# Performance work log

Hardware: AMD Instinct MI355X
Metric: run time of the kernel (lower is better)

The kernel has to match this reference:

```python
import jax, jax.numpy as jnp
import numpy as np

N, E = 50000, 800000
HID, HEADS, EDIM = 64, 4, 32
HC = HID * HEADS
NEG_SLOPE = 0.2
LN_EPS = 1e-5


def setup_inputs() -> dict:
    key = jax.random.key(0)
    ks = jax.random.split(key, 16)
    s = lambda d: 1.0 / np.sqrt(d)
    return {
        "x": jax.random.normal(ks[0], (N, HID), jnp.float32),
        "edge_index": jax.random.randint(ks[1], (2, E), 0, N, jnp.int64),
        "edge_attr": jax.random.normal(ks[2], (E, EDIM), jnp.float32),
        # GATv2Conv params
        "W_l": jax.random.normal(ks[3], (HID, HC), jnp.float32) * s(HID),
        "b_l": jnp.zeros((HC,), jnp.float32),
        "W_r": jax.random.normal(ks[4], (HID, HC), jnp.float32) * s(HID),
        "b_r": jnp.zeros((HC,), jnp.float32),
        "W_e": jax.random.normal(ks[5], (EDIM, HC), jnp.float32) * s(EDIM),
        "att": jax.random.normal(ks[6], (HEADS, HID), jnp.float32) * s(HID),
        "bias_gat": jnp.zeros((HC,), jnp.float32),
        # block params
        "W1": jax.random.normal(ks[7], (HID, HC), jnp.float32) * s(HID),
        "b1": jnp.zeros((HC,), jnp.float32),
        "gamma": jnp.ones((HC,), jnp.float32),
        "beta": jnp.zeros((HC,), jnp.float32),
        "W2": jax.random.normal(ks[8], (HC, HID), jnp.float32) * s(HC),
        "b2": jnp.zeros((HID,), jnp.float32),
    }


def _gatv2(x, edge_index, edge_attr, W_l, b_l, W_r, b_r, W_e, att, bias_gat):
    src, dst = edge_index[0], edge_index[1]
    x_l = (x @ W_l + b_l).reshape(N, HEADS, HID)  # source transform
    x_r = (x @ W_r + b_r).reshape(N, HEADS, HID)  # target transform
    e = (edge_attr @ W_e).reshape(E, HEADS, HID)
    m = x_l[src] + x_r[dst] + e                    # [E, H, C]
    m = jax.nn.leaky_relu(m, NEG_SLOPE)
    alpha = jnp.einsum('ehc,hc->eh', m, att)       # [E, H]
    # segment softmax over incoming edges of each target node
    amax = jax.ops.segment_max(alpha, dst, num_segments=N)
    alpha = jnp.exp(alpha - amax[dst])
    denom = jax.ops.segment_sum(alpha, dst, num_segments=N)
    alpha = alpha / (denom[dst] + 1e-16)
    out = jax.ops.segment_sum(x_l[src] * alpha[..., None], dst, num_segments=N)
    return out.reshape(N, HC) + bias_gat


def reference(x, edge_index, edge_attr, W_l, b_l, W_r, b_r, W_e, att, bias_gat,
              W1, b1, gamma, beta, W2, b2):
    h = _gatv2(x, edge_index, edge_attr, W_l, b_l, W_r, b_r, W_e, att, bias_gat)
    xl = jnp.tanh(x @ W1 + b1)
    z = xl + h
    mu = jnp.mean(z, axis=-1, keepdims=True)
    var = jnp.var(z, axis=-1, keepdims=True)
    z = (z - mu) * jax.lax.rsqrt(var + LN_EPS) * gamma + beta
    return jnp.tanh(z @ W2 + b2)
```

## Files before the change

kernel.cpp:

```cpp
#include <hip/hip_runtime.h>
#include <math.h>

#define N_NODES 50000
#define N_EDGES 800000
#define HID 64
#define HEADS 4
#define HC 256
#define NEG_SLOPE 0.2f
#define LN_EPS 1e-5f
#define EDGE_BLOCKS 2048

typedef __attribute__((ext_vector_type(8))) short bf16x8;
typedef __attribute__((ext_vector_type(8))) unsigned short u16x8;
typedef __attribute__((ext_vector_type(4))) float f32x4;

__device__ __forceinline__ float bf2f(unsigned short u) {
    return __uint_as_float(((unsigned int)u) << 16);
}
__device__ __forceinline__ unsigned short f2bf(float f) {
    unsigned int u = __float_as_uint(f);
    u = (u + 0x7fffu + ((u >> 16) & 1u)) >> 16;
    return (unsigned short)u;
}
__device__ __forceinline__ float fast_tanh(float v) {
    const float c = fminf(fmaxf(v, -15.f), 15.f);
    const float e = __expf(2.f * c);
    return 1.f - 2.f / (e + 1.f);
}

__global__ __launch_bounds__(256) void k_node_transform(
    const float* __restrict__ x,
    const float* __restrict__ W_l, const float* __restrict__ b_l,
    const float* __restrict__ W_r, const float* __restrict__ b_r,
    unsigned short* __restrict__ xl_t, unsigned short* __restrict__ xr_t)
{
    __shared__ float xs[8][64];
    __shared__ unsigned short tl[8][256], tr[8][256];
    const int n0 = blockIdx.x * 8;
    const int t = threadIdx.x;
    for (int i = t; i < 8 * 64; i += 256) xs[i >> 6][i & 63] = x[n0 * 64 + i];
    __syncthreads();

    float accl[8], accr[8];
    const float bl = b_l[t], br = b_r[t];
#pragma unroll
    for (int n = 0; n < 8; n++) { accl[n] = bl; accr[n] = br; }
    for (int k = 0; k < 64; k++) {
        const float wl = W_l[k * 256 + t];
        const float wr = W_r[k * 256 + t];
#pragma unroll
        for (int n = 0; n < 8; n++) {
            accl[n] = fmaf(xs[n][k], wl, accl[n]);
            accr[n] = fmaf(xs[n][k], wr, accr[n]);
        }
    }
    const int pos = (t & 15) * 16 + (t >> 4);
#pragma unroll
    for (int n = 0; n < 8; n++) {
        tl[n][pos] = f2bf(accl[n]);
        tr[n][pos] = f2bf(accr[n]);
    }
    __syncthreads();
    const int n = t >> 5, q = t & 31;
    ushort4 v0 = *(const ushort4*)&tl[n][q * 8];
    ushort4 v1 = *(const ushort4*)&tl[n][q * 8 + 4];
    ushort4 w0 = *(const ushort4*)&tr[n][q * 8];
    ushort4 w1 = *(const ushort4*)&tr[n][q * 8 + 4];
    *(ushort4*)(xl_t + (size_t)(n0 + n) * 256 + q * 8)     = v0;
    *(ushort4*)(xl_t + (size_t)(n0 + n) * 256 + q * 8 + 4) = v1;
    *(ushort4*)(xr_t + (size_t)(n0 + n) * 256 + q * 8)     = w0;
    *(ushort4*)(xr_t + (size_t)(n0 + n) * 256 + q * 8 + 4) = w1;
}

__global__ __launch_bounds__(256) void k_prep(
    const float* __restrict__ W_e, const float* __restrict__ att,
    unsigned short* __restrict__ wfrag, unsigned short* __restrict__ att_t)
{
    const int t = threadIdx.x;
#pragma unroll
    for (int s = 0; s < 4; s++) {
        const int slot = t * 4 + s;
        const int nt = slot >> 6, ls = slot & 63;
        const int col = nt * 16 + (ls & 15);
        const int kb = (ls >> 4) * 8;
#pragma unroll
        for (int j = 0; j < 8; j++)
            wfrag[slot * 8 + j] = f2bf(W_e[(kb + j) * 256 + col]);
    }
    att_t[t] = f2bf(att[(t & 15) * 16 + (t >> 4)]);
}

__global__ __launch_bounds__(256) void k_hist(const int* __restrict__ ei, int* __restrict__ count)
{
    const int e = blockIdx.x * 256 + threadIdx.x;
    if (e < N_EDGES) atomicAdd(&count[ei[N_EDGES + e]], 1);
}

__global__ __launch_bounds__(1024) void k_scan(const int* __restrict__ count, int* __restrict__ off)
{
    __shared__ int wsum[16];
    __shared__ int s_carry;
    const int t = threadIdx.x, lane = t & 63, wv = t >> 6;
    if (t == 0) s_carry = 0;
    __syncthreads();
    for (int base = 0; base < N_NODES; base += 8192) {
        const int idx0 = base + t * 8;
        int v[8];
#pragma unroll
        for (int j = 0; j < 8; j++) { int i = idx0 + j; v[j] = (i < N_NODES) ? count[i] : 0; }
#pragma unroll
        for (int j = 1; j < 8; j++) v[j] += v[j - 1];
        const int tot = v[7];
        int sc = tot;
#pragma unroll
        for (int s = 1; s < 64; s <<= 1) { int o = __shfl_up(sc, s, 64); if (lane >= s) sc += o; }
        if (lane == 63) wsum[wv] = sc;
        __syncthreads();
        const int carry = s_carry;
        int woff = 0;
        for (int u = 0; u < wv; u++) woff += wsum[u];
        const int ebase = carry + woff + (sc - tot);
#pragma unroll
        for (int j = 0; j < 8; j++) {
            int i = idx0 + j;
            if (i < N_NODES) off[i] = ebase + (j ? v[j - 1] : 0);
        }
        __syncthreads();
        if (t == 0) { int tt = 0; for (int u = 0; u < 16; u++) tt += wsum[u]; s_carry = carry + tt; }
        __syncthreads();
    }
    if (threadIdx.x == 0) off[N_NODES] = s_carry;
}

__global__ __launch_bounds__(256) void k_scatter(
    const int* __restrict__ ei, const int* __restrict__ off, int* __restrict__ cursor,
    const float* __restrict__ edge_attr,
    int* __restrict__ csr_src, unsigned short* __restrict__ ea_csr)
{
    const int e = blockIdx.x * 256 + threadIdx.x;
    if (e < N_EDGES) {
        const int s = ei[e];
        const int d = ei[N_EDGES + e];
        const int pos = off[d] + atomicAdd(&cursor[d], 1);
        csr_src[pos] = s;
        const float4* src4 = (const float4*)(edge_attr + (size_t)e * 32);
        ushort4* dst4 = (ushort4*)(ea_csr + (size_t)pos * 32);
#pragma unroll
        for (int i = 0; i < 8; i++) {
            const float4 v = src4[i];
            ushort4 u;
            u.x = f2bf(v.x); u.y = f2bf(v.y); u.z = f2bf(v.z); u.w = f2bf(v.w);
            dst4[i] = u;
        }
    }
}

template<bool F32>
__global__ __launch_bounds__(256) void k_edgeagg(
    const int* __restrict__ off, const int* __restrict__ csr_src,
    const unsigned short* __restrict__ ea_csr,
    const unsigned short* __restrict__ wfrag, const unsigned short* __restrict__ att_t,
    const unsigned short* __restrict__ xl_t, const unsigned short* __restrict__ xr_t,
    void* __restrict__ zs_g)
{
    __shared__ unsigned short bfrag_s[16][64][8];

    const int t = threadIdx.x;
    const int lane = t & 63, wv = t >> 6;
    const int arow = lane & 15, koct = lane >> 4;

    for (int i = t; i < 1024; i += 256)
        *(u16x8*)&bfrag_s[i >> 6][i & 63][0] = *(const u16x8*)(wfrag + i * 8);
    __syncthreads();

    const u16x8 attL = *(const u16x8*)(att_t + arow * 16);
    const u16x8 attH = *(const u16x8*)(att_t + arow * 16 + 8);

    const int STRIDE = EDGE_BLOCKS * 4;
    int node = blockIdx.x * 4 + wv;
    if (node >= N_NODES) return;

    int lo = off[node], hi = off[node + 1];
    u16x8 xrl = *(const u16x8*)(xr_t + (size_t)node * 256 + arow * 16);
    u16x8 xrh = *(const u16x8*)(xr_t + (size_t)node * 256 + arow * 16 + 8);
    while (hi <= lo) {
#pragma unroll
        for (int q = 0; q < 4; q++) {
            const int nt = koct * 4 + q;
            if (F32) ((float*)zs_g)[(size_t)node * 256 + nt * 16 + arow] = 0.f;
            else ((unsigned short*)zs_g)[(size_t)node * 256 + nt * 16 + arow] = 0;
        }
        node += STRIDE;
        if (node >= N_NODES) return;
        lo = off[node]; hi = off[node + 1];
        xrl = *(const u16x8*)(xr_t + (size_t)node * 256 + arow * 16);
        xrh = *(const u16x8*)(xr_t + (size_t)node * 256 + arow * 16 + 8);
    }
    int nnode = node + STRIDE;
    bool nvalid = nnode < N_NODES;
    int nlo = 0, nhi = 0;
    u16x8 nxrl = xrl, nxrh = xrh;
    if (nvalid) {
        nlo = off[nnode]; nhi = off[nnode + 1];
        nxrl = *(const u16x8*)(xr_t + (size_t)nnode * 256 + arow * 16);
        nxrh = *(const u16x8*)(xr_t + (size_t)nnode * 256 + arow * 16 + 8);
    }
    int p0 = lo;
    bf16x8 af;
    u16x8 xlo[4], xhi[4];
    {
        const int pa = min(p0 + arow, hi - 1);
        const int sv0 = csr_src[pa];
        af = *(const bf16x8*)(ea_csr + (size_t)pa * 32 + koct * 8);
#pragma unroll
        for (int r = 0; r < 4; r++) {
            const int sr = __shfl(sv0, koct * 4 + r, 64);
            const unsigned short* bp = xl_t + (size_t)sr * 256 + arow * 16;
            xlo[r] = *(const u16x8*)bp;
            xhi[r] = *(const u16x8*)(bp + 8);
        }
    }

    float g[16];
#pragma unroll
    for (int i = 0; i < 16; i++) g[i] = 0.f;
    float dsum[4] = {0.f, 0.f, 0.f, 0.f};

    for (;;) {
        const bool last = (p0 + 16 >= hi);
        bool uvalid;
        int up0, uhic;
        if (!last) { uvalid = true; up0 = p0 + 16; uhic = hi; }
        else {
            while (nvalid && nlo >= nhi) {
#pragma unroll
                for (int q = 0; q < 4; q++) {
                    const int nt = koct * 4 + q;
                    if (F32) ((float*)zs_g)[(size_t)nnode * 256 + nt * 16 + arow] = 0.f;
                    else ((unsigned short*)zs_g)[(size_t)nnode * 256 + nt * 16 + arow] = 0;
                }
                nnode += STRIDE;
                nvalid = nnode < N_NODES;
                if (nvalid) {
                    nlo = off[nnode]; nhi = off[nnode + 1];
                    nxrl = *(const u16x8*)(xr_t + (size_t)nnode * 256 + arow * 16);
                    nxrh = *(const u16x8*)(xr_t + (size_t)nnode * 256 + arow * 16 + 8);
                }
            }
            uvalid = nvalid; up0 = nlo; uhic = nhi;
        }
        int usv = 0;
        bf16x8 uaf = af;
        if (uvalid) {
            const int upa = min(up0 + arow, uhic - 1);
            usv = csr_src[upa];
            uaf = *(const bf16x8*)(ea_csr + (size_t)upa * 32 + koct * 8);
        }

        float s_[4][4];
#pragma unroll
        for (int r = 0; r < 4; r++)
#pragma unroll
            for (int h = 0; h < 4; h++) s_[r][h] = 0.f;

#pragma unroll
        for (int nt = 0; nt < 8; nt++) {
            const bf16x8 bfr = *(const bf16x8*)&bfrag_s[nt][lane][0];
            f32x4 dacc = {0.f, 0.f, 0.f, 0.f};
            dacc = __builtin_amdgcn_mfma_f32_16x16x32_bf16(af, bfr, dacc, 0, 0, 0);
            const float xrv = bf2f((unsigned short)xrl[nt]);
            const float atv = bf2f((unsigned short)attL[nt]);
            const int h = nt >> 2;
#pragma unroll
            for (int r = 0; r < 4; r++) {
                const float xv = bf2f((unsigned short)xlo[r][nt]);
                float mm = dacc[r] + xv + xrv;
                mm = (mm > 0.f) ? mm : NEG_SLOPE * mm;
                s_[r][h] = fmaf(atv, mm, s_[r][h]);
            }
        }
        u16x8 uxlo[4], uxhi[4];
        if (uvalid) {
#pragma unroll
            for (int r = 0; r < 4; r++) {
                const int sr = __shfl(usv, koct * 4 + r, 64);
                const unsigned short* bp = xl_t + (size_t)sr * 256 + arow * 16;
                uxlo[r] = *(const u16x8*)bp;
                uxhi[r] = *(const u16x8*)(bp + 8);
            }
        } else {
#pragma unroll
            for (int r = 0; r < 4; r++) { uxlo[r] = xlo[r]; uxhi[r] = xhi[r]; }
        }
#pragma unroll
        for (int n2 = 0; n2 < 8; n2++) {
            const int nt = n2 + 8;
            const bf16x8 bfr = *(const bf16x8*)&bfrag_s[nt][lane][0];
            f32x4 dacc = {0.f, 0.f, 0.f, 0.f};
            dacc = __builtin_amdgcn_mfma_f32_16x16x32_bf16(af, bfr, dacc, 0, 0, 0);
            const float xrv = bf2f((unsigned short)xrh[n2]);
            const float atv = bf2f((unsigned short)attH[n2]);
            const int h = nt >> 2;
#pragma unroll
            for (int r = 0; r < 4; r++) {
                const float xv = bf2f((unsigned short)xhi[r][n2]);
                float mm = dacc[r] + xv + xrv;
                mm = (mm > 0.f) ? mm : NEG_SLOPE * mm;
                s_[r][h] = fmaf(atv, mm, s_[r][h]);
            }
        }
#pragma unroll
        for (int r = 0; r < 4; r++)
#pragma unroll
            for (int h = 0; h < 4; h++) {
                float v = s_[r][h];
                v += __shfl_xor(v, 1, 64);
                v += __shfl_xor(v, 2, 64);
                v += __shfl_xor(v, 4, 64);
                v += __shfl_xor(v, 8, 64);
                s_[r][h] = v;
            }
#pragma unroll
        for (int h = 0; h < 4; h++) {
            float w4[4];
#pragma unroll
            for (int r = 0; r < 4; r++) {
                const bool ok = (p0 + koct * 4 + r) < hi;
                w4[r] = ok ? __expf(fminf(s_[r][h], 60.f)) : 0.f;
            }
            dsum[h] += (w4[0] + w4[1]) + (w4[2] + w4[3]);
#pragma unroll
            for (int q = 0; q < 4; q++) {
                const int nt = h * 4 + q;
                float acc = g[nt];
#pragma unroll
                for (int r = 0; r < 4; r++) {
                    const float xv = bf2f((unsigned short)(nt < 8 ? xlo[r][nt & 7] : xhi[r][nt & 7]));
                    acc = fmaf(w4[r], xv, acc);
                }
                g[nt] = acc;
            }
        }

        if (last) {
#pragma unroll
            for (int i = 0; i < 16; i++) {
                float v = g[i];
                v += __shfl_xor(v, 16, 64);
                v += __shfl_xor(v, 32, 64);
                g[i] = v;
            }
#pragma unroll
            for (int h = 0; h < 4; h++) {
                float v = dsum[h];
                v += __shfl_xor(v, 16, 64);
                v += __shfl_xor(v, 32, 64);
                dsum[h] = v;
            }
            float inv[4];
#pragma unroll
            for (int h = 0; h < 4; h++) inv[h] = 1.f / (dsum[h] + 1e-16f);
#pragma unroll
            for (int q = 0; q < 4; q++) {
                const int nt = koct * 4 + q;
                const float v = g[nt] * inv[nt >> 2];
                if (F32) ((float*)zs_g)[(size_t)node * 256 + nt * 16 + arow] = v;
                else ((unsigned short*)zs_g)[(size_t)node * 256 + nt * 16 + arow] = f2bf(v);
            }
            if (!uvalid) return;
            node = nnode; lo = nlo; hi = nhi; xrl = nxrl; xrh = nxrh;
#pragma unroll
            for (int i = 0; i < 16; i++) g[i] = 0.f;
#pragma unroll
            for (int h = 0; h < 4; h++) dsum[h] = 0.f;
            nnode += STRIDE;
            nvalid = nnode < N_NODES;
            if (nvalid) {
                nlo = off[nnode]; nhi = off[nnode + 1];
                nxrl = *(const u16x8*)(xr_t + (size_t)nnode * 256 + arow * 16);
                nxrh = *(const u16x8*)(xr_t + (size_t)nnode * 256 + arow * 16 + 8);
            }
        }
        p0 = up0;
        af = uaf;
#pragma unroll
        for (int r = 0; r < 4; r++) { xlo[r] = uxlo[r]; xhi[r] = uxhi[r]; }
    }
}

template<bool F32>
__global__ __launch_bounds__(256) void k_post(
    const void* __restrict__ zs_g, const float* __restrict__ x,
    const float* __restrict__ bias_gat,
    const float* __restrict__ W1, const float* __restrict__ b1,
    const float* __restrict__ gamma, const float* __restrict__ beta,
    const float* __restrict__ W2, const float* __restrict__ b2,
    float* __restrict__ out)
{
    __shared__ float xs[16][64];
    __shared__ float zsh[16][256];
    __shared__ float part[16][4][64];
    __shared__ float redS[16][4], redQ[16][4];

    const int n0 = blockIdx.x * 16;
    const int t = threadIdx.x, lane = t & 63, wv = t >> 6;

    for (int i = t; i < 16 * 64; i += 256) xs[i >> 6][i & 63] = x[n0 * 64 + i];
    __syncthreads();

    float a1[16];
    const float b1v = b1[t];
#pragma unroll
    for (int n = 0; n < 16; n++) a1[n] = b1v;
    for (int k = 0; k < 64; k++) {
        const float w1v = W1[k * 256 + t];
#pragma unroll
        for (int n = 0; n < 16; n++) a1[n] = fmaf(xs[n][k], w1v, a1[n]);
    }

    const float bg = bias_gat[t];
    float z[16];
#pragma unroll
    for (int n = 0; n < 16; n++) {
        const float gv = F32 ? ((const float*)zs_g)[(size_t)(n0 + n) * 256 + t]
                             : bf2f(((const unsigned short*)zs_g)[(size_t)(n0 + n) * 256 + t]);
        z[n] = fast_tanh(a1[n]) + gv + bg;
    }

    const float gm = gamma[t], bt = beta[t];
#pragma unroll
    for (int n = 0; n < 16; n++) {
        float s = z[n], q = z[n] * z[n];
#pragma unroll
        for (int m = 1; m < 64; m <<= 1) { s += __shfl_xor(s, m, 64); q += __shfl_xor(q, m, 64); }
        if (lane == 0) { redS[n][wv] = s; redQ[n][wv] = q; }
    }
    __syncthreads();
#pragma unroll
    for (int n = 0; n < 16; n++) {
        const float s = redS[n][0] + redS[n][1] + redS[n][2] + redS[n][3];
        const float q = redQ[n][0] + redQ[n][1] + redQ[n][2] + redQ[n][3];
        const float mu = s * (1.f / 256.f);
        const float var = q * (1.f / 256.f) - mu * mu;
        const float ivn = rsqrtf(var + LN_EPS);
        zsh[n][t] = (z[n] - mu) * ivn * gm + bt;
    }
    __syncthreads();

    const int j = t & 63, qq = t >> 6;
    float p[16];
#pragma unroll
    for (int n = 0; n < 16; n++) p[n] = 0.f;
    for (int c0 = 0; c0 < 64; c0++) {
        const int c = qq * 64 + c0;
        const float w2v = W2[c * 64 + j];
#pragma unroll
        for (int n = 0; n < 16; n++) p[n] = fmaf(zsh[n][c], w2v, p[n]);
    }
#pragma unroll
    for (int n = 0; n < 16; n++) part[n][qq][j] = p[n];
    __syncthreads();
#pragma unroll
    for (int i = 0; i < 4; i++) {
        const int n = wv * 4 + i;
        const float s = part[n][0][lane] + part[n][1][lane] + part[n][2][lane] + part[n][3][lane];
        out[(size_t)(n0 + n) * 64 + lane] = fast_tanh(s + b2[lane]);
    }
}

extern "C" void kernel_launch(void* const* d_in, const int* in_sizes, int n_in,
                              void* d_out, int out_size, void* d_ws, size_t ws_size,
                              hipStream_t stream)
{
    const float* x         = (const float*)d_in[0];
    const int*   ei        = (const int*)d_in[1];
    const float* edge_attr = (const float*)d_in[2];
    const float* W_l       = (const float*)d_in[3];
    const float* b_l       = (const float*)d_in[4];
    const float* W_r       = (const float*)d_in[5];
    const float* b_r       = (const float*)d_in[6];
    const float* W_e       = (const float*)d_in[7];
    const float* att       = (const float*)d_in[8];
    const float* bias_gat  = (const float*)d_in[9];
    const float* W1        = (const float*)d_in[10];
    const float* b1        = (const float*)d_in[11];
    const float* gamma     = (const float*)d_in[12];
    const float* beta      = (const float*)d_in[13];
    const float* W2        = (const float*)d_in[14];
    const float* b2        = (const float*)d_in[15];
    float* out = (float*)d_out;

    char* wsb = (char*)d_ws;
    size_t o = 0;
    unsigned short* xl_t   = (unsigned short*)(wsb + o);  o += (size_t)N_NODES * HC * 2;
    unsigned short* xr_t   = (unsigned short*)(wsb + o);  o += (size_t)N_NODES * HC * 2;
    unsigned short* ea_csr = (unsigned short*)(wsb + o);  o += (size_t)N_EDGES * 32 * 2;
    int* csr_src           = (int*)(wsb + o);             o += (size_t)N_EDGES * 4;
    int* count             = (int*)(wsb + o);             o += (size_t)N_NODES * 4;
    int* cursor            = (int*)(wsb + o);             o += (size_t)N_NODES * 4;
    int* off               = (int*)(wsb + o);             o += (size_t)(N_NODES + 1) * 4;
    unsigned short* wfrag  = (unsigned short*)(wsb + o);  o += 16 * 64 * 8 * 2;
    unsigned short* att_t  = (unsigned short*)(wsb + o);  o += 256 * 2;
    o = (o + 255) & ~(size_t)255;
    void* zs_g             = (void*)(wsb + o);
    const bool f32ok = (o + (size_t)N_NODES * HC * 4) <= ws_size;

    hipMemsetAsync(count, 0, 2 * (size_t)N_NODES * sizeof(int), stream);

    k_node_transform<<<N_NODES / 8, 256, 0, stream>>>(x, W_l, b_l, W_r, b_r, xl_t, xr_t);
    k_prep<<<1, 256, 0, stream>>>(W_e, att, wfrag, att_t);
    k_hist<<<(N_EDGES + 255) / 256, 256, 0, stream>>>(ei, count);
    k_scan<<<1, 1024, 0, stream>>>(count, off);
    k_scatter<<<(N_EDGES + 255) / 256, 256, 0, stream>>>(ei, off, cursor, edge_attr,
                                                         csr_src, ea_csr);
    if (f32ok) {
        k_edgeagg<true><<<EDGE_BLOCKS, 256, 0, stream>>>(off, csr_src, ea_csr, wfrag, att_t,
                                                         xl_t, xr_t, zs_g);
        k_post<true><<<N_NODES / 16, 256, 0, stream>>>(zs_g, x, bias_gat,
                                                       W1, b1, gamma, beta, W2, b2, out);
    } else {
        k_edgeagg<false><<<EDGE_BLOCKS, 256, 0, stream>>>(off, csr_src, ea_csr, wfrag, att_t,
                                                          xl_t, xr_t, zs_g);
        k_post<false><<<N_NODES / 16, 256, 0, stream>>>(zs_g, x, bias_gat,
                                                        W1, b1, gamma, beta, W2, b2, out);
    }
}
```

Before: 616.9 us.

## Batch CSR source-index loads per wave, fold xr into MFMA accumulator init

The edge-aggregation kernel now loads up to 64 source indices per wave in one coalesced read and serves later 16-edge chunks from registers through shuffles, refreshing only every 32 edges, instead of issuing a csr_src load per chunk. The x_r term is used as the MFMA accumulator's initial value, and leaky-relu becomes a single fmaxf, removing a few VALU ops per element. The node-transform kernel processes 16 nodes per block instead of 8, reusing each weight load twice as often at the cost of more registers. The shuffle-window bookkeeping is subtle and wrong indexing would silently corrupt the result.

```diff
diff --git a/kernel.cpp b/kernel.cpp
--- a/kernel.cpp
+++ b/kernel.cpp
@@ -34,42 +34,39 @@
     const float* __restrict__ W_r, const float* __restrict__ b_r,
     unsigned short* __restrict__ xl_t, unsigned short* __restrict__ xr_t)
 {
-    __shared__ float xs[8][64];
-    __shared__ unsigned short tl[8][256], tr[8][256];
-    const int n0 = blockIdx.x * 8;
+    __shared__ float xs[16][64];
+    __shared__ unsigned short tl[16][256], tr[16][256];
+    const int n0 = blockIdx.x * 16;
     const int t = threadIdx.x;
-    for (int i = t; i < 8 * 64; i += 256) xs[i >> 6][i & 63] = x[n0 * 64 + i];
-    __syncthreads();
-
-    float accl[8], accr[8];
+    for (int i = t; i < 16 * 64; i += 256) xs[i >> 6][i & 63] = x[n0 * 64 + i];
+    __syncthreads();
+
+    float accl[16], accr[16];
     const float bl = b_l[t], br = b_r[t];
 #pragma unroll
-    for (int n = 0; n < 8; n++) { accl[n] = bl; accr[n] = br; }
+    for (int n = 0; n < 16; n++) { accl[n] = bl; accr[n] = br; }
     for (int k = 0; k < 64; k++) {
         const float wl = W_l[k * 256 + t];
         const float wr = W_r[k * 256 + t];
 #pragma unroll
-        for (int n = 0; n < 8; n++) {
+        for (int n = 0; n < 16; n++) {
             accl[n] = fmaf(xs[n][k], wl, accl[n]);
             accr[n] = fmaf(xs[n][k], wr, accr[n]);
         }
     }
     const int pos = (t & 15) * 16 + (t >> 4);
 #pragma unroll
-    for (int n = 0; n < 8; n++) {
+    for (int n = 0; n < 16; n++) {
         tl[n][pos] = f2bf(accl[n]);
         tr[n][pos] = f2bf(accr[n]);
     }
     __syncthreads();
-    const int n = t >> 5, q = t & 31;
-    ushort4 v0 = *(const ushort4*)&tl[n][q * 8];
-    ushort4 v1 = *(const ushort4*)&tl[n][q * 8 + 4];
-    ushort4 w0 = *(const ushort4*)&tr[n][q * 8];
-    ushort4 w1 = *(const ushort4*)&tr[n][q * 8 + 4];
-    *(ushort4*)(xl_t + (size_t)(n0 + n) * 256 + q * 8)     = v0;
-    *(ushort4*)(xl_t + (size_t)(n0 + n) * 256 + q * 8 + 4) = v1;
-    *(ushort4*)(xr_t + (size_t)(n0 + n) * 256 + q * 8)     = w0;
-    *(ushort4*)(xr_t + (size_t)(n0 + n) * 256 + q * 8 + 4) = w1;
+    const int n = t >> 4, q = t & 15;
+#pragma unroll
+    for (int i = 0; i < 4; i++) {
+        *(ushort4*)(xl_t + (size_t)(n0 + n) * 256 + q * 16 + i * 4) = *(const ushort4*)&tl[n][q * 16 + i * 4];
+        *(ushort4*)(xr_t + (size_t)(n0 + n) * 256 + q * 16 + i * 4) = *(const ushort4*)&tr[n][q * 16 + i * 4];
+    }
 }
 
 __global__ __launch_bounds__(256) void k_prep(
@@ -196,25 +193,27 @@
         xrl = *(const u16x8*)(xr_t + (size_t)node * 256 + arow * 16);
         xrh = *(const u16x8*)(xr_t + (size_t)node * 256 + arow * 16 + 8);
     }
+    int svbase = lo;
+    int svall = csr_src[min(svbase + lane, hi - 1)];
+
     int nnode = node + STRIDE;
     bool nvalid = nnode < N_NODES;
-    int nlo = 0, nhi = 0;
+    int nlo = 0, nhi = 0, nsvall = 0;
     u16x8 nxrl = xrl, nxrh = xrh;
     if (nvalid) {
         nlo = off[nnode]; nhi = off[nnode + 1];
         nxrl = *(const u16x8*)(xr_t + (size_t)nnode * 256 + arow * 16);
         nxrh = *(const u16x8*)(xr_t + (size_t)nnode * 256 + arow * 16 + 8);
+        if (nhi > nlo) nsvall = csr_src[min(nlo + lane, nhi - 1)];
     }
     int p0 = lo;
     bf16x8 af;
     u16x8 xlo[4], xhi[4];
     {
-        const int pa = min(p0 + arow, hi - 1);
-        const int sv0 = csr_src[pa];
-        af = *(const bf16x8*)(ea_csr + (size_t)pa * 32 + koct * 8);
+        af = *(const bf16x8*)(ea_csr + (size_t)min(p0 + arow, hi - 1) * 32 + koct * 8);
 #pragma unroll
         for (int r = 0; r < 4; r++) {
-            const int sr = __shfl(sv0, koct * 4 + r, 64);
+            const int sr = __shfl(svall, koct * 4 + r, 64);
             const unsigned short* bp = xl_t + (size_t)sr * 256 + arow * 16;
             xlo[r] = *(const u16x8*)bp;
             xhi[r] = *(const u16x8*)(bp + 8);
@@ -245,17 +244,14 @@
                     nlo = off[nnode]; nhi = off[nnode + 1];
                     nxrl = *(const u16x8*)(xr_t + (size_t)nnode * 256 + arow * 16);
                     nxrh = *(const u16x8*)(xr_t + (size_t)nnode * 256 + arow * 16 + 8);
+                    if (nhi > nlo) nsvall = csr_src[min(nlo + lane, nhi - 1)];
                 }
             }
             uvalid = nvalid; up0 = nlo; uhic = nhi;
         }
-        int usv = 0;
         bf16x8 uaf = af;
-        if (uvalid) {
-            const int upa = min(up0 + arow, uhic - 1);
-            usv = csr_src[upa];
-            uaf = *(const bf16x8*)(ea_csr + (size_t)upa * 32 + koct * 8);
-        }
+        if (uvalid)
+            uaf = *(const bf16x8*)(ea_csr + (size_t)min(up0 + arow, uhic - 1) * 32 + koct * 8);
 
         float s_[4][4];
 #pragma unroll
@@ -266,24 +262,25 @@
 #pragma unroll
         for (int nt = 0; nt < 8; nt++) {
             const bf16x8 bfr = *(const bf16x8*)&bfrag_s[nt][lane][0];
-            f32x4 dacc = {0.f, 0.f, 0.f, 0.f};
+            const float xrv = bf2f((unsigned short)xrl[nt]);
+            f32x4 dacc = {xrv, xrv, xrv, xrv};
             dacc = __builtin_amdgcn_mfma_f32_16x16x32_bf16(af, bfr, dacc, 0, 0, 0);
-            const float xrv = bf2f((unsigned short)xrl[nt]);
             const float atv = bf2f((unsigned short)attL[nt]);
             const int h = nt >> 2;
 #pragma unroll
             for (int r = 0; r < 4; r++) {
-                const float xv = bf2f((unsigned short)xlo[r][nt]);
-                float mm = dacc[r] + xv + xrv;
-                mm = (mm > 0.f) ? mm : NEG_SLOPE * mm;
-                s_[r][h] = fmaf(atv, mm, s_[r][h]);
+                const float mm = dacc[r] + bf2f((unsigned short)xlo[r][nt]);
+                const float lk = fmaxf(mm, NEG_SLOPE * mm);
+                s_[r][h] = fmaf(atv, lk, s_[r][h]);
             }
         }
         u16x8 uxlo[4], uxhi[4];
         if (uvalid) {
+            const int ubase = last ? 0 : (up0 - svbase);
+            const int usrcv = last ? nsvall : svall;
 #pragma unroll
             for (int r = 0; r < 4; r++) {
-                const int sr = __shfl(usv, koct * 4 + r, 64);
+                const int sr = __shfl(usrcv, ubase + koct * 4 + r, 64);
                 const unsigned short* bp = xl_t + (size_t)sr * 256 + arow * 16;
                 uxlo[r] = *(const u16x8*)bp;
                 uxhi[r] = *(const u16x8*)(bp + 8);
@@ -296,17 +293,16 @@
         for (int n2 = 0; n2 < 8; n2++) {
             const int nt = n2 + 8;
             const bf16x8 bfr = *(const bf16x8*)&bfrag_s[nt][lane][0];
-            f32x4 dacc = {0.f, 0.f, 0.f, 0.f};
+            const float xrv = bf2f((unsigned short)xrh[n2]);
+            f32x4 dacc = {xrv, xrv, xrv, xrv};
             dacc = __builtin_amdgcn_mfma_f32_16x16x32_bf16(af, bfr, dacc, 0, 0, 0);
-            const float xrv = bf2f((unsigned short)xrh[n2]);
             const float atv = bf2f((unsigned short)attH[n2]);
             const int h = nt >> 2;
 #pragma unroll
             for (int r = 0; r < 4; r++) {
-                const float xv = bf2f((unsigned short)xhi[r][n2]);
-                float mm = dacc[r] + xv + xrv;
-                mm = (mm > 0.f) ? mm : NEG_SLOPE * mm;
-                s_[r][h] = fmaf(atv, mm, s_[r][h]);
+                const float mm = dacc[r] + bf2f((unsigned short)xhi[r][n2]);
+                const float lk = fmaxf(mm, NEG_SLOPE * mm);
+                s_[r][h] = fmaf(atv, lk, s_[r][h]);
             }
         }
 #pragma unroll
@@ -369,6 +365,7 @@
             }
             if (!uvalid) return;
             node = nnode; lo = nlo; hi = nhi; xrl = nxrl; xrh = nxrh;
+            svbase = nlo; svall = nsvall;
 #pragma unroll
             for (int i = 0; i < 16; i++) g[i] = 0.f;
 #pragma unroll
@@ -379,12 +376,17 @@
                 nlo = off[nnode]; nhi = off[nnode + 1];
                 nxrl = *(const u16x8*)(xr_t + (size_t)nnode * 256 + arow * 16);
                 nxrh = *(const u16x8*)(xr_t + (size_t)nnode * 256 + arow * 16 + 8);
+                if (nhi > nlo) nsvall = csr_src[min(nlo + lane, nhi - 1)];
             }
         }
         p0 = up0;
         af = uaf;
 #pragma unroll
         for (int r = 0; r < 4; r++) { xlo[r] = uxlo[r]; xhi[r] = uxhi[r]; }
+        if (p0 - svbase >= 32) {
+            svbase = p0;
+            svall = csr_src[min(svbase + lane, hi - 1)];
+        }
     }
 }
 
@@ -507,7 +509,7 @@
 
     hipMemsetAsync(count, 0, 2 * (size_t)N_NODES * sizeof(int), stream);
 
-    k_node_transform<<<N_NODES / 8, 256, 0, stream>>>(x, W_l, b_l, W_r, b_r, xl_t, xr_t);
+    k_node_transform<<<N_NODES / 16, 256, 0, stream>>>(x, W_l, b_l, W_r, b_r, xl_t, xr_t);
     k_prep<<<1, 256, 0, stream>>>(W_e, att, wfrag, att_t);
     k_hist<<<(N_EDGES + 255) / 256, 256, 0, stream>>>(ei, count);
     k_scan<<<1, 1024, 0, stream>>>(count, off);
```

Result: faster. 598.1 us (-3.0%).
